# Kernel tuning notes

Hardware: AMD Instinct MI355X
Metric: run time of the kernel (lower is better)

Reference implementation:

```python
import jax, jax.numpy as jnp
import numpy as np

# ---- DNC configuration (mirrors access_config / controller_config / args) ----
T, B, IN, OUT = 64, 32, 64, 64          # time, batch, input_size, output_size
N, Wd, R, NW = 128, 64, 4, 1            # memory_size, word_size, num_reads, num_writes
H = 256                                  # controller hidden_size (2 LSTM layers)
CLIP = 20.0
EPS = 1e-6
NUM_MODES = 2 * NW + 1                   # backward modes, forward modes, content mode
IF_SIZES = [R*Wd, R, NW*Wd, NW, NW*Wd, NW*Wd, R, NW, NW, R*NUM_MODES]
IF_SIZE = int(np.sum(IF_SIZES))


def setup_inputs() -> dict:
    key = jax.random.key(0)
    ks = jax.random.split(key, 12)
    in0 = IN + R * Wd  # controller input = external input + flattened prev reads

    def w(k, shape, fan):
        return jax.random.normal(k, shape, jnp.float32) / np.float32(np.sqrt(fan))

    return {
        "inputs": jax.random.normal(ks[0], (T, B, IN), jnp.float32),
        "Wx0": w(ks[1], (in0, 4 * H), in0),
        "Wh0": w(ks[2], (H, 4 * H), H),
        "b0": jnp.zeros((4 * H,), jnp.float32),
        "Wx1": w(ks[3], (H, 4 * H), H),
        "Wh1": w(ks[4], (H, 4 * H), H),
        "b1": jnp.zeros((4 * H,), jnp.float32),
        "W_if": w(ks[5], (H, IF_SIZE), H),
        "b_if": jnp.zeros((IF_SIZE,), jnp.float32),
        "W_out": w(ks[6], (H + R * Wd, OUT), H + R * Wd),
        "b_out": jnp.zeros((OUT,), jnp.float32),
    }


def _lstm(x, h, c, Wx, Wh, b):
    g = x @ Wx + h @ Wh + b
    i, f, gg, o = jnp.split(g, 4, axis=-1)
    c2 = jax.nn.sigmoid(f) * c + jax.nn.sigmoid(i) * jnp.tanh(gg)
    h2 = jax.nn.sigmoid(o) * jnp.tanh(c2)
    return h2, c2


def _content_weights(memory, keys, strengths):
    # memory [B,N,W], keys [B,h,W], strengths [B,h] -> [B,h,N]
    mnorm = jnp.linalg.norm(memory, axis=-1)          # [B,N]
    knorm = jnp.linalg.norm(keys, axis=-1)            # [B,h]
    dot = jnp.einsum('bhw,bnw->bhn', keys, memory)
    sim = dot / (knorm[..., None] * mnorm[:, None, :] + EPS)
    return jax.nn.softmax(sim * strengths[..., None], axis=-1)


def _allocation(usage):
    # usage [B,N] -> allocation weighting [B,N] (DNC freeness-based)
    usage = EPS + (1.0 - EPS) * usage
    order = jnp.argsort(usage, axis=-1)               # ascending usage (most free first)
    sorted_usage = jnp.take_along_axis(usage, order, axis=-1)
    prod = jnp.cumprod(sorted_usage, axis=-1)
    prod_excl = jnp.concatenate([jnp.ones_like(prod[:, :1]), prod[:, :-1]], axis=-1)
    alloc_sorted = (1.0 - sorted_usage) * prod_excl
    inv = jnp.argsort(order, axis=-1)
    return jnp.take_along_axis(alloc_sorted, inv, axis=-1)


def _dnc_forward(inputs, Wx0, Wh0, b0, Wx1, Wh1, b1, W_if, b_if, W_out, b_out):
    eye = 1.0 - jnp.eye(N, dtype=jnp.float32)
    splits = np.cumsum(IF_SIZES)[:-1]

    def step(state, x_t):
        h0, c0, h1, c1, M, rw, ww, link, prec, usage, reads = state
        ctrl_in = jnp.concatenate([x_t, reads.reshape(B, R * Wd)], axis=-1)
        h0, c0 = _lstm(ctrl_in, h0, c0, Wx0, Wh0, b0)
        h1, c1 = _lstm(h0, h1, c1, Wx1, Wh1, b1)
        ctrl = jnp.clip(h1, -CLIP, CLIP)

        p = jnp.split(ctrl @ W_if + b_if, splits, axis=-1)
        read_keys = p[0].reshape(B, R, Wd)
        read_str = 1.0 + jax.nn.softplus(p[1])              # oneplus
        write_keys = p[2].reshape(B, NW, Wd)
        write_str = 1.0 + jax.nn.softplus(p[3])
        erase = jax.nn.sigmoid(p[4]).reshape(B, NW, Wd)
        write_vec = p[5].reshape(B, NW, Wd)
        free_g = jax.nn.sigmoid(p[6])                       # [B,R]
        alloc_g = jax.nn.sigmoid(p[7])                      # [B,NW]
        write_g = jax.nn.sigmoid(p[8])                      # [B,NW]
        modes = jax.nn.softmax(p[9].reshape(B, R, NUM_MODES), axis=-1)

        # -- usage update (prev write weights, then free gates on prev reads) --
        cw = 1.0 - jnp.prod(1.0 - ww, axis=1)               # [B,N]
        u = usage + (1.0 - usage) * cw
        psi = jnp.prod(1.0 - free_g[..., None] * rw, axis=1)
        usage = u * psi

        # -- write weights: content + allocation, gated --
        wc = _content_weights(M, write_keys, write_str)     # [B,NW,N]
        u_tmp = usage
        ww_heads = []
        for i in range(NW):
            a = _allocation(u_tmp)
            wg = write_g[:, i:i+1]
            ag = alloc_g[:, i:i+1]
            ww_heads.append(wg * (ag * a + (1.0 - ag) * wc[:, i]))
            u_tmp = u_tmp + (1.0 - u_tmp) * wg * a
        ww = jnp.stack(ww_heads, axis=1)                    # [B,NW,N]

        # -- erase + write memory --
        erase_m = jnp.prod(1.0 - ww[..., None] * erase[:, :, None, :], axis=1)  # [B,N,W]
        add_m = jnp.einsum('bwn,bwk->bnk', ww, write_vec)
        M = M * erase_m + add_m

        # -- temporal link matrix + precedence --
        wi = ww[..., :, None]
        wj = ww[..., None, :]
        link = ((1.0 - wi - wj) * link + wi * prec[..., None, :]) * eye
        prec = (1.0 - ww.sum(axis=-1, keepdims=True)) * prec + ww

        # -- read weights: backward / content / forward modes --
        rc = _content_weights(M, read_keys, read_str)       # [B,R,N]
        fwd = jnp.einsum('bwij,brj->brwi', link, rw)
        bwd = jnp.einsum('bwji,brj->brwi', link, rw)
        bmode = modes[..., :NW]
        fmode = modes[..., NW:2*NW]
        cmode = modes[..., 2*NW]
        rw = (jnp.einsum('brw,brwn->brn', bmode, bwd)
              + cmode[..., None] * rc
              + jnp.einsum('brw,brwn->brn', fmode, fwd))
        reads = jnp.einsum('brn,bnk->brk', rw, M)           # [B,R,W]

        out = jnp.clip(jnp.concatenate([ctrl, reads.reshape(B, R * Wd)], axis=-1) @ W_out + b_out,
                       -CLIP, CLIP)
        return (h0, c0, h1, c1, M, rw, ww, link, prec, usage, reads), out

    z = jnp.zeros
    init = (z((B, H)), z((B, H)), z((B, H)), z((B, H)),
            z((B, N, Wd)), z((B, R, N)), z((B, NW, N)),
            z((B, NW, N, N)), z((B, NW, N)), z((B, N)), z((B, R, Wd)))
    _, outs = jax.lax.scan(step, init, inputs)
    return outs                                            # [T,B,OUT]


def reference(inputs, Wx0, Wh0, b0, Wx1, Wh1, b1, W_if, b_if, W_out, b_out):
    return _dnc_forward(inputs, Wx0, Wh0, b0, Wx1, Wh1, b1, W_if, b_if, W_out, b_out)
```

## Files before the change

kernel.cpp:

```cpp
#include <hip/hip_runtime.h>
#include <math.h>


#define TT   64
#define BB   32
#define INW  64
#define OUTW 64
#define NN   128
#define WD   64
#define RR   4
#define HH   256
#define IFSZ 471
#define CLIPV 20.0f
#define EPSV  1e-6f
#define NBLK 96

#define OFF_RK   0
#define OFF_RSTR 256
#define OFF_WK   260
#define OFF_WSTR 324
#define OFF_ER   325
#define OFF_WV   389
#define OFF_FG   453
#define OFF_AG   457
#define OFF_WG   458
#define OFF_MD   459

#define S_WSTR 0
#define S_AG   1
#define S_WG   2
#define S_KNW  3
#define S_WSUM 4
#define S_RSTR 8
#define S_FG   12
#define S_KNR  16
#define S_BM   20
#define S_FM   24
#define S_CM   28

#define A_XS   0
#define A_GL   11840
#define A_C0   12896
#define A_GO   13152
#define A_WS   13216
#define A_WO   34528
#define B_XS   0
#define B_GL   9472
#define B_C1   10528
#define B_W1   10784
#define C_MS   0
#define C_LS   8320
#define C_WW   24832
#define C_PRC  24960
#define C_USG  25088
#define C_RWS  25216
#define C_IFC  25728
#define C_FWD  26208
#define C_BWD  26720
#define C_U2   27232
#define C_WCS  27360
#define C_RCS  27488
#define C_MNO  28000
#define C_RDS  28128
#define C_ERS  28384
#define C_WVS  28448
#define C_SC   28512
#define C_SCAL 28576

#define SMEM_FLOATS 36064
#define SMEM_BYTES  (SMEM_FLOATS*4)

#define W_CTL  0
#define W_RDS  8192
#define W_H0   16384
#define W_H1   32768
#define W_FLA  49152
#define W_FLB  (W_FLA + 1024)
#define W_FLC  (W_FLB + 1024)
#define W_END  (W_FLC + 1024)

__device__ __forceinline__ float sigf(float x){ return 1.0f/(1.0f+expf(-x)); }
__device__ __forceinline__ float sofp(float x){ return fmaxf(x,0.0f)+log1pf(expf(-fabsf(x))); }

__device__ __forceinline__ float gload(const float* p){
  return __hip_atomic_load(p, __ATOMIC_RELAXED, __HIP_MEMORY_SCOPE_AGENT);
}
__device__ __forceinline__ void gstore(float* p, float v){
  __hip_atomic_store(p, v, __ATOMIC_RELAXED, __HIP_MEMORY_SCOPE_AGENT);
}

__device__ __forceinline__ void waitflag(const unsigned* slots, unsigned target){
  if (threadIdx.x < 64){
    for (;;){
      unsigned m = __hip_atomic_load(&slots[(threadIdx.x & 31)*32],
                                     __ATOMIC_RELAXED, __HIP_MEMORY_SCOPE_AGENT);
      #pragma unroll
      for (int s=32;s>0;s>>=1){
        unsigned o = (unsigned)__shfl_xor((int)m, s, 64);
        m = (o < m) ? o : m;
      }
      if (m >= target) break;
      __builtin_amdgcn_s_sleep(2);
    }
  }
  __syncthreads();
}

__device__ __forceinline__ void setflag(unsigned* slots, int g, unsigned val){
  asm volatile("s_waitcnt vmcnt(0)" ::: "memory");
  __syncthreads();
  if (threadIdx.x == 0)
    __hip_atomic_store(&slots[g*32], val, __ATOMIC_RELAXED, __HIP_MEMORY_SCOPE_AGENT);
}

__device__ __forceinline__ float wredSum(float v){
  #pragma unroll
  for (int m=32;m>0;m>>=1) v += __shfl_xor(v,m,64);
  return v;
}
__device__ __forceinline__ float wredMax(float v){
  #pragma unroll
  for (int m=32;m>0;m>>=1) v = fmaxf(v,__shfl_xor(v,m,64));
  return v;
}

__device__ __forceinline__ float bfly64(float (&A)[64], int l, int* jb){
  #pragma unroll
  for (int st=0; st<6; ++st){
    const int m = 1<<st, half = 32>>st;
    const bool hi = (l & m) != 0;
    #pragma unroll
    for (int j=0;j<half;j++){
      float a = A[j], b = A[j+half];
      float keep = hi? b : a;
      float send = hi? a : b;
      A[j] = keep + __shfl_xor(send, m, 64);
    }
  }
  *jb = ((l&1)?32:0)|((l&2)?16:0)|((l&4)?8:0)|((l&8)?4:0)|((l&16)?2:0)|((l&32)?1:0);
  return A[0];
}

#define TILE_FMA(WBASE, WROW, XROW)                                      \
  {                                                                      \
    float xv[8], wv[8];                                                  \
    _Pragma("unroll")                                                    \
    for (int q=0;q<8;q++){                                               \
      wv[q] = sm[(WBASE) + (WROW)*37 + c0 + q];                          \
      xv[q] = Xs[(XROW)*37 + b0 + q];                                    \
    }                                                                    \
    _Pragma("unroll")                                                    \
    for (int bi=0;bi<8;bi++)                                             \
      _Pragma("unroll")                                                  \
      for (int ci=0;ci<8;ci++)                                           \
        acc[bi*8+ci] += xv[bi]*wv[ci];                                   \
  }

extern "C" __global__ __launch_bounds__(1024, 1)
void dnc_coop11(const float* __restrict__ inputs,
                const float* __restrict__ Wx0, const float* __restrict__ Wh0, const float* __restrict__ b0g,
                const float* __restrict__ Wx1, const float* __restrict__ Wh1, const float* __restrict__ b1g,
                const float* __restrict__ Wifg, const float* __restrict__ bifg,
                const float* __restrict__ Woutg, const float* __restrict__ boutg,
                float* __restrict__ outg, float* __restrict__ ws)
{
  const int bid  = blockIdx.x;
  const int role = bid >> 5;
  const int g    = bid & 31;
  const int tid  = threadIdx.x;
  const int lane = tid & 63;
  const int wid  = tid >> 6;

  extern __shared__ float sm[];

  float* gctl  = ws + W_CTL;
  float* greads= ws + W_RDS;
  unsigned* fA = (unsigned*)(ws + W_FLA);
  unsigned* fB = (unsigned*)(ws + W_FLB);
  unsigned* fC = (unsigned*)(ws + W_FLC);

  if (role == 0){
    for (int i = tid; i < 576*32; i += 1024){
      int r = i >> 5, cl = i & 31;
      int cglob = 8*g + (cl&7) + ((cl>>3)<<8);
      float v;
      if (r < 256)      v = Wx0[(64+r)*1024 + cglob];
      else if (r < 320) v = Wx0[(r-256)*1024 + cglob];
      else              v = Wh0[(r-320)*1024 + cglob];
      sm[A_WS + r*37 + cl] = v;
    }
    for (int i = tid; i < 512*2; i += 1024){
      int k = i >> 1, c = i & 1;
      sm[A_WO + k*3 + c] = Woutg[k*64 + 2*g + c];
    }
    if (tid < 256) sm[A_C0 + tid] = 0.0f;
  } else if (role == 1){
    for (int i = tid; i < 512*32; i += 1024){
      int r = i >> 5, cl = i & 31;
      int cglob = 8*g + (cl&7) + ((cl>>3)<<8);
      sm[B_W1 + r*37 + cl] = (r < 256) ? Wx1[r*1024 + cglob]
                                       : Wh1[(r-256)*1024 + cglob];
    }
    if (tid < 256) sm[B_C1 + tid] = 0.0f;
  } else {
    for (int i = tid; i < NN*65;  i += 1024) sm[C_MS + i] = 0.0f;
    for (int i = tid; i < NN*129; i += 1024) sm[C_LS + i] = 0.0f;
    if (tid < 128){ sm[C_WW+tid]=0.f; sm[C_PRC+tid]=0.f; sm[C_USG+tid]=0.f; }
    if (tid < 512) sm[C_RWS+tid]=0.f;
  }
  __syncthreads();

  if (role == 0){
    float* Xs = sm + A_XS;
    for (int t = 0; t <= TT; ++t){
      float* h0old = ws + W_H0 + (t&1)*8192;
      float* h0new = ws + W_H0 + ((t+1)&1)*8192;
      float acc[64]; float accO[16];

      waitflag(fA, (unsigned)t);
      if (t < TT){
        for (int i = tid; i < 256*32; i += 1024){
          int k = i>>5, bb = i&31; Xs[k*37+bb] = gload(&h0old[i]);
        }
        for (int i = tid; i < 64*32; i += 1024){
          int bb = i>>6, k = i&63;
          Xs[(256+k)*37+bb] = inputs[(t*BB + bb)*INW + k];
        }
        __syncthreads();
        #pragma unroll
        for (int j=0;j<64;j++) acc[j]=0.f;
        {
          const int b0 = (wid>>2)*8, c0 = (wid&3)*8;
          #pragma unroll
          for (int i=0;i<4;i++){
            int k = i*64 + lane;
            TILE_FMA(A_WS, 320+k, k)
          }
          TILE_FMA(A_WS, 256+lane, 256+lane)
        }
        __syncthreads();
      }
      if (t > 0){
        waitflag(fB, (unsigned)t);
        for (int i = tid; i < 256*32; i += 1024){
          int k = i>>5, bb = i&31; Xs[k*37+bb] = gload(&gctl[i]);
        }
        __syncthreads();
        #pragma unroll
        for (int j=0;j<16;j++) accO[j]=0.f;
        if (wid < 4){
          const int b0 = wid*8;
          #pragma unroll
          for (int i=0;i<4;i++){
            int k = i*64 + lane;
            float w0 = sm[A_WO + k*3], w1 = sm[A_WO + k*3 + 1];
            float xv[8];
            #pragma unroll
            for (int q=0;q<8;q++) xv[q] = Xs[k*37 + b0 + q];
            #pragma unroll
            for (int bi=0;bi<8;bi++){
              accO[bi*2]   += xv[bi]*w0;
              accO[bi*2+1] += xv[bi]*w1;
            }
          }
        }
        __syncthreads();
      }
      waitflag(fC, (unsigned)t);
      for (int i = tid; i < 256*32; i += 1024){
        int k = i>>5, bb = i&31; Xs[k*37+bb] = gload(&greads[i]);
      }
      __syncthreads();
      if (t < TT){
        {
          const int b0 = (wid>>2)*8, c0 = (wid&3)*8;
          #pragma unroll
          for (int i=0;i<4;i++){
            int k = i*64 + lane;
            TILE_FMA(A_WS, k, k)
          }
          int jb; float v = bfly64(acc, lane, &jb);
          sm[A_GL + (b0 + (jb>>3))*33 + c0 + (jb&7)] = v;
        }
        __syncthreads();
        if (tid < 256){
          int j = tid>>5, bb = tid&31;
          float gi = sm[A_GL + bb*33 + j]      + b0g[8*g + j];
          float gf = sm[A_GL + bb*33 + 8 + j]  + b0g[256 + 8*g + j];
          float gg = sm[A_GL + bb*33 + 16 + j] + b0g[512 + 8*g + j];
          float go = sm[A_GL + bb*33 + 24 + j] + b0g[768 + 8*g + j];
          float c = sigf(gf)*sm[A_C0 + j*32 + bb] + sigf(gi)*tanhf(gg);
          sm[A_C0 + j*32 + bb] = c;
          gstore(&h0new[256*g + tid], sigf(go)*tanhf(c));
        }
        setflag(fA, g, (unsigned)(t+1));
      }
      if (t > 0){
        if (wid < 4){
          const int b0 = wid*8;
          #pragma unroll
          for (int i=0;i<4;i++){
            int k = i*64 + lane;
            float w0 = sm[A_WO + (256+k)*3], w1 = sm[A_WO + (256+k)*3 + 1];
            float xv[8];
            #pragma unroll
            for (int q=0;q<8;q++) xv[q] = Xs[k*37 + b0 + q];
            #pragma unroll
            for (int bi=0;bi<8;bi++){
              accO[bi*2]   += xv[bi]*w0;
              accO[bi*2+1] += xv[bi]*w1;
            }
          }
          #pragma unroll
          for (int st=0; st<4; ++st){
            const int m = 1<<st, half = 8>>st;
            const bool hi = (lane & m) != 0;
            #pragma unroll
            for (int j=0;j<half;j++){
              float a = accO[j], b = accO[j+half];
              float keep = hi? b : a;
              float send = hi? a : b;
              accO[j] = keep + __shfl_xor(send, m, 64);
            }
          }
          accO[0] += __shfl_xor(accO[0], 16, 64);
          accO[0] += __shfl_xor(accO[0], 32, 64);
          int jb = ((lane&1)?8:0)|((lane&2)?4:0)|((lane&4)?2:0)|((lane&8)?1:0);
          if ((lane & 48) == 0){
            int bi = jb>>1, ci = jb&1;
            sm[A_GO + (wid*8+bi)*2 + ci] = accO[0];
          }
        }
        __syncthreads();
        if (tid < 64){
          int bb = tid>>1, c = tid&1;
          float v = sm[A_GO + tid] + boutg[2*g + c];
          outg[((t-1)*BB + bb)*OUTW + 2*g + c] = fminf(CLIPV, fmaxf(-CLIPV, v));
        }
      }
    }
  } else if (role == 1){
    float* Xs = sm + B_XS;
    for (int t = 0; t < TT; ++t){
      float* h0new = ws + W_H0 + ((t+1)&1)*8192;
      float* h1old = ws + W_H1 + (t&1)*8192;
      float* h1new = ws + W_H1 + ((t+1)&1)*8192;
      float acc[64];
      #pragma unroll
      for (int j=0;j<64;j++) acc[j]=0.f;

      waitflag(fB, (unsigned)t);
      for (int i = tid; i < 256*32; i += 1024){
        int k = i>>5, bb = i&31; Xs[k*37+bb] = gload(&h1old[i]);
      }
      __syncthreads();
      {
        const int b0 = (wid>>2)*8, c0 = (wid&3)*8;
        #pragma unroll
        for (int i=0;i<4;i++){
          int k = i*64 + lane;
          TILE_FMA(B_W1, 256+k, k)
        }
      }
      __syncthreads();
      waitflag(fA, (unsigned)(t+1));
      for (int i = tid; i < 256*32; i += 1024){
        int k = i>>5, bb = i&31; Xs[k*37+bb] = gload(&h0new[i]);
      }
      __syncthreads();
      {
        const int b0 = (wid>>2)*8, c0 = (wid&3)*8;
        #pragma unroll
        for (int i=0;i<4;i++){
          int k = i*64 + lane;
          TILE_FMA(B_W1, k, k)
        }
        int jb; float v = bfly64(acc, lane, &jb);
        sm[B_GL + (b0 + (jb>>3))*33 + c0 + (jb&7)] = v;
      }
      __syncthreads();
      if (tid < 256){
        int j = tid>>5, bb = tid&31;
        float gi = sm[B_GL + bb*33 + j]      + b1g[8*g + j];
        float gf = sm[B_GL + bb*33 + 8 + j]  + b1g[256 + 8*g + j];
        float gg = sm[B_GL + bb*33 + 16 + j] + b1g[512 + 8*g + j];
        float go = sm[B_GL + bb*33 + 24 + j] + b1g[768 + 8*g + j];
        float c = sigf(gf)*sm[B_C1 + j*32 + bb] + sigf(gi)*tanhf(gg);
        sm[B_C1 + j*32 + bb] = c;
        float h = sigf(go)*tanhf(c);
        gstore(&h1new[256*g + tid], h);
        gstore(&gctl[256*g + tid], fminf(CLIPV, fmaxf(-CLIPV, h)));
      }
      setflag(fB, g, (unsigned)(t+1));
    }
  } else {
    float* Ms  = sm + C_MS;
    float* Ls  = sm + C_LS;
    float* wws = sm + C_WW;
    float* prc = sm + C_PRC;
    float* usg = sm + C_USG;
    float* rws = sm + C_RWS;
    float* ifcl= sm + C_IFC;
    float* fwds= sm + C_FWD;
    float* bwds= sm + C_BWD;
    float* u2  = sm + C_U2;
    float* wcs = sm + C_WCS;
    float* rcs = sm + C_RCS;
    float* mno = sm + C_MNO;
    float* ers = sm + C_ERS;
    float* wvs = sm + C_WVS;
    float* sc  = sm + C_SC;
    float* scal= sm + C_SCAL;
    float* ctl_l = sm + C_RCS;
    float* part  = sm + C_FWD;

    for (int t = 0; t < TT; ++t){
      if (tid < 128){
        float s=0.f;
        #pragma unroll 8
        for (int d=0;d<WD;d++){ float v=Ms[tid*65+d]; s+=v*v; }
        mno[tid]=sqrtf(s);
      }
      waitflag(fB, (unsigned)(t+1));
      if (tid < 256) ctl_l[tid] = gload(&gctl[tid*32 + g]);
      __syncthreads();
      {
        const int kq = tid >> 9, c = tid & 511;
        if (c < IFSZ){
          const float* Wp = Wifg + (size_t)(kq*128)*IFSZ + c;
          const float* xp = ctl_l + kq*128;
          float a0=0.f, a1=0.f;
          #pragma unroll 8
          for (int k=0;k<128;k+=2){
            a0 += xp[k]   * Wp[(size_t)k*IFSZ];
            a1 += xp[k+1] * Wp[(size_t)(k+1)*IFSZ];
          }
          part[kq*512 + c] = a0 + a1;
        }
      }
      __syncthreads();
      if (tid < IFSZ) ifcl[tid] = part[tid] + part[512+tid] + bifg[tid];
      __syncthreads();

      if (tid < RR){
        scal[S_RSTR+tid]=1.0f+sofp(ifcl[OFF_RSTR+tid]);
        scal[S_FG+tid]  =sigf(ifcl[OFF_FG+tid]);
        float m0=ifcl[OFF_MD+tid*3], m1=ifcl[OFF_MD+tid*3+1], m2=ifcl[OFF_MD+tid*3+2];
        float mx=fmaxf(m0,fmaxf(m1,m2));
        float e0=expf(m0-mx), e1=expf(m1-mx), e2=expf(m2-mx);
        float s=e0+e1+e2;
        scal[S_BM+tid]=e0/s; scal[S_FM+tid]=e1/s; scal[S_CM+tid]=e2/s;
      }
      if (tid == 4) scal[S_WSTR]=1.0f+sofp(ifcl[OFF_WSTR]);
      if (tid == 5) scal[S_AG]=sigf(ifcl[OFF_AG]);
      if (tid == 6) scal[S_WG]=sigf(ifcl[OFF_WG]);
      if (tid >= 64 && tid < 128){
        int d=tid-64;
        ers[d]=sigf(ifcl[OFF_ER+d]);
        wvs[d]=ifcl[OFF_WV+d];
      }
      if (wid == 8){
        float v=ifcl[OFF_WK+lane]; float s=wredSum(v*v);
        if (lane==0) scal[S_KNW]=sqrtf(s);
      }
      if (wid >= 10 && wid < 14){
        int r=wid-10; float v=ifcl[OFF_RK+r*WD+lane]; float s=wredSum(v*v);
        if (lane==0) scal[S_KNR+r]=sqrtf(s);
      }
      __syncthreads();
      if (tid < NN){
        float dot=0.f;
        #pragma unroll 8
        for (int d=0;d<WD;d++) dot += ifcl[OFF_WK+d]*Ms[tid*65+d];
        float sim = dot/(scal[S_KNW]*mno[tid]+EPSV);
        wcs[tid]=sim*scal[S_WSTR];
      }
      __syncthreads();
      if (tid < NN){ float mx=wredMax(wcs[tid]); if(lane==0) sc[wid]=mx; }
      __syncthreads();
      if (tid < NN){
        float mx=fmaxf(sc[0],sc[1]);
        float e=expf(wcs[tid]-mx);
        wcs[tid]=e;
        float s=wredSum(e); if(lane==0) sc[2+wid]=s;
      }
      __syncthreads();
      if (tid < NN) wcs[tid]=wcs[tid]/(sc[2]+sc[3]);
      __syncthreads();
      if (tid < NN){
        float cw = wws[tid];
        float u  = usg[tid] + (1.0f-usg[tid])*cw;
        float psi=1.0f;
        #pragma unroll
        for (int r=0;r<RR;r++) psi *= 1.0f - scal[S_FG+r]*rws[r*NN+tid];
        float us = u*psi;
        usg[tid]=us;
        u2[tid] = EPSV + (1.0f-EPSV)*us;
      }
      __syncthreads();
      if (tid < NN){
        float ui=u2[tid]; float p=1.0f;
        for (int j=0;j<NN;j++){
          float uj=u2[j];
          bool take = (uj<ui) || (uj==ui && j<tid);
          p *= take ? uj : 1.0f;
        }
        float a = (1.0f-ui)*p;
        float wwn = scal[S_WG]*( scal[S_AG]*a + (1.0f-scal[S_AG])*wcs[tid] );
        wws[tid]=wwn;
        float s=wredSum(wwn); if(lane==0) sc[wid]=s;
      }
      __syncthreads();
      if (tid==0) scal[S_WSUM]=sc[0]+sc[1];
      __syncthreads();
      #pragma unroll
      for (int i=0;i<8;i++){
        int el=tid+i*1024, n=el>>6, d=el&63;
        float w=wws[n];
        Ms[n*65+d] = Ms[n*65+d]*(1.0f - w*ers[d]) + w*wvs[d];
      }
      #pragma unroll
      for (int i=0;i<16;i++){
        int el=tid+i*1024, li=el>>7, lj=el&127;
        float v = (li==lj) ? 0.0f
                : (1.0f - wws[li] - wws[lj])*Ls[li*129+lj] + wws[li]*prc[lj];
        Ls[li*129+lj]=v;
      }
      __syncthreads();
      if (tid < NN) prc[tid] = (1.0f - scal[S_WSUM])*prc[tid] + wws[tid];
      if (tid >= 128 && tid < 256){
        int n=tid-128; float s=0.f;
        #pragma unroll 8
        for (int d=0;d<WD;d++){ float v=Ms[n*65+d]; s+=v*v; }
        mno[n]=sqrtf(s);
      }
      __syncthreads();
      if (tid < RR*NN){
        int r=tid>>7, n=tid&127;
        float dot=0.f;
        #pragma unroll 8
        for (int d=0;d<WD;d++) dot += ifcl[OFF_RK+r*WD+d]*Ms[n*65+d];
        float sim = dot/(scal[S_KNR+r]*mno[n]+EPSV);
        rcs[tid]=sim*scal[S_RSTR+r];
      }
      __syncthreads();
      if (tid < RR*NN){ float mx=wredMax(rcs[tid]); if(lane==0) sc[wid]=mx; }
      __syncthreads();
      if (tid < RR*NN){
        int r=tid>>7;
        float mx=fmaxf(sc[r*2],sc[r*2+1]);
        float e=expf(rcs[tid]-mx);
        rcs[tid]=e;
        float s=wredSum(e); if(lane==0) sc[8+wid]=s;
      }
      __syncthreads();
      if (tid < RR*NN){
        int r=tid>>7;
        rcs[tid]=rcs[tid]/(sc[8+r*2]+sc[9+r*2]);
      }
      __syncthreads();
      if (tid < RR*NN){
        int r=tid>>7, i=tid&127;
        float f=0.f, bw=0.f;
        const float* rwr = rws + r*NN;
        #pragma unroll 4
        for (int j=0;j<NN;j++){
          float rv=rwr[j];
          f  += Ls[i*129+j]*rv;
          bw += Ls[j*129+i]*rv;
        }
        fwds[tid]=f; bwds[tid]=bw;
      }
      __syncthreads();
      if (tid < RR*NN){
        int r=tid>>7;
        rws[tid] = scal[S_BM+r]*bwds[tid] + scal[S_CM+r]*rcs[tid] + scal[S_FM+r]*fwds[tid];
      }
      __syncthreads();
      if (tid < RR*WD){
        int r=tid>>6, d=tid&63;
        float s=0.f;
        #pragma unroll 8
        for (int n=0;n<NN;n++) s += rws[r*NN+n]*Ms[n*65+d];
        gstore(&greads[tid*32 + g], s);
      }
      setflag(fC, g, (unsigned)(t+1));
    }
  }
}

extern "C" void kernel_launch(void* const* d_in, const int* in_sizes, int n_in,
                              void* d_out, int out_size, void* d_ws, size_t ws_size,
                              hipStream_t stream)
{
  const float* inputs=(const float*)d_in[0];
  const float* Wx0   =(const float*)d_in[1];
  const float* Wh0   =(const float*)d_in[2];
  const float* b0    =(const float*)d_in[3];
  const float* Wx1   =(const float*)d_in[4];
  const float* Wh1   =(const float*)d_in[5];
  const float* b1    =(const float*)d_in[6];
  const float* Wif   =(const float*)d_in[7];
  const float* bif   =(const float*)d_in[8];
  const float* Wout  =(const float*)d_in[9];
  const float* bout  =(const float*)d_in[10];
  float* out = (float*)d_out;
  float* ws  = (float*)d_ws;

  hipMemsetAsync(ws, 0, W_END * sizeof(float), stream);

  hipFuncSetAttribute((const void*)dnc_coop11,
                      hipFuncAttributeMaxDynamicSharedMemorySize, SMEM_BYTES);

  void* args[] = { (void*)&inputs, (void*)&Wx0, (void*)&Wh0, (void*)&b0,
                   (void*)&Wx1, (void*)&Wh1, (void*)&b1, (void*)&Wif,
                   (void*)&bif, (void*)&Wout, (void*)&bout, (void*)&out,
                   (void*)&ws };
  hipLaunchCooperativeKernel((void*)dnc_coop11, dim3(NBLK), dim3(1024),
                             args, SMEM_BYTES, stream);
}
```

Measured before the change: 3.135 ms.

## Merge memory-stage phases to cut barriers and rebalance per-step work

Restructures the per-timestep memory block. It splits the interface matvec into four k-quarters over all 1024 threads. The usage update now runs alongside write content scoring, and the read content scoring (with the memory norm fused in) runs concurrently with the link forward/backward products. The softmax normalisations are folded into their consumers, and the final read-vector reduction is split four ways over all threads. The aim is to remove many __syncthreads phases and idle threads on the serial critical path, at the cost of an extra reduction buffer and some redundant norm computation.

```diff
diff --git a/kernel.cpp b/kernel.cpp
--- a/kernel.cpp
+++ b/kernel.cpp
@@ -30,7 +30,6 @@
 #define S_AG   1
 #define S_WG   2
 #define S_KNW  3
-#define S_WSUM 4
 #define S_RSTR 8
 #define S_FG   12
 #define S_KNR  16
@@ -61,11 +60,11 @@
 #define C_WCS  27360
 #define C_RCS  27488
 #define C_MNO  28000
-#define C_RDS  28128
 #define C_ERS  28384
 #define C_WVS  28448
 #define C_SC   28512
 #define C_SCAL 28576
+#define C_PART2 28608
 
 #define SMEM_FLOATS 36064
 #define SMEM_BYTES  (SMEM_FLOATS*4)
@@ -157,7 +156,7 @@
   }
 
 extern "C" __global__ __launch_bounds__(1024, 1)
-void dnc_coop11(const float* __restrict__ inputs,
+void dnc_coop12(const float* __restrict__ inputs,
                 const float* __restrict__ Wx0, const float* __restrict__ Wh0, const float* __restrict__ b0g,
                 const float* __restrict__ Wx1, const float* __restrict__ Wh1, const float* __restrict__ b1g,
                 const float* __restrict__ Wifg, const float* __restrict__ bifg,
@@ -412,7 +411,7 @@
     float* sc  = sm + C_SC;
     float* scal= sm + C_SCAL;
     float* ctl_l = sm + C_RCS;
-    float* part  = sm + C_FWD;
+    float* part2 = sm + C_PART2;
 
     for (int t = 0; t < TT; ++t){
       if (tid < 128){
@@ -425,21 +424,24 @@
       if (tid < 256) ctl_l[tid] = gload(&gctl[tid*32 + g]);
       __syncthreads();
       {
-        const int kq = tid >> 9, c = tid & 511;
-        if (c < IFSZ){
-          const float* Wp = Wifg + (size_t)(kq*128)*IFSZ + c;
-          const float* xp = ctl_l + kq*128;
-          float a0=0.f, a1=0.f;
-          #pragma unroll 8
-          for (int k=0;k<128;k+=2){
-            a0 += xp[k]   * Wp[(size_t)k*IFSZ];
-            a1 += xp[k+1] * Wp[(size_t)(k+1)*IFSZ];
-          }
-          part[kq*512 + c] = a0 + a1;
-        }
-      }
-      __syncthreads();
-      if (tid < IFSZ) ifcl[tid] = part[tid] + part[512+tid] + bifg[tid];
+        const int kq = tid >> 8, c = tid & 255;
+        const int c2 = c + 256;
+        const bool has2 = (c2 < IFSZ);
+        const float* Wp = Wifg + (size_t)(kq*64)*IFSZ;
+        const float* xp = ctl_l + kq*64;
+        float a0=0.f, a1=0.f;
+        #pragma unroll 8
+        for (int k=0;k<64;k++){
+          float x = xp[k];
+          a0 += x * Wp[(size_t)k*IFSZ + c];
+          if (has2) a1 += x * Wp[(size_t)k*IFSZ + c2];
+        }
+        part2[kq*512 + c] = a0;
+        if (has2) part2[kq*512 + c2] = a1;
+      }
+      __syncthreads();
+      if (tid < IFSZ)
+        ifcl[tid] = part2[tid] + part2[512+tid] + part2[1024+tid] + part2[1536+tid] + bifg[tid];
       __syncthreads();
 
       if (tid < RR){
@@ -468,12 +470,22 @@
         if (lane==0) scal[S_KNR+r]=sqrtf(s);
       }
       __syncthreads();
+
       if (tid < NN){
         float dot=0.f;
         #pragma unroll 8
         for (int d=0;d<WD;d++) dot += ifcl[OFF_WK+d]*Ms[tid*65+d];
-        float sim = dot/(scal[S_KNW]*mno[tid]+EPSV);
-        wcs[tid]=sim*scal[S_WSTR];
+        wcs[tid] = dot/(scal[S_KNW]*mno[tid]+EPSV)*scal[S_WSTR];
+      } else if (tid < 256){
+        int n = tid-128;
+        float cw = wws[n];
+        float u  = usg[n] + (1.0f-usg[n])*cw;
+        float psi=1.0f;
+        #pragma unroll
+        for (int r=0;r<RR;r++) psi *= 1.0f - scal[S_FG+r]*rws[r*NN+n];
+        float us = u*psi;
+        usg[n]=us;
+        u2[n] = EPSV + (1.0f-EPSV)*us;
       }
       __syncthreads();
       if (tid < NN){ float mx=wredMax(wcs[tid]); if(lane==0) sc[wid]=mx; }
@@ -485,20 +497,8 @@
         float s=wredSum(e); if(lane==0) sc[2+wid]=s;
       }
       __syncthreads();
-      if (tid < NN) wcs[tid]=wcs[tid]/(sc[2]+sc[3]);
-      __syncthreads();
       if (tid < NN){
-        float cw = wws[tid];
-        float u  = usg[tid] + (1.0f-usg[tid])*cw;
-        float psi=1.0f;
-        #pragma unroll
-        for (int r=0;r<RR;r++) psi *= 1.0f - scal[S_FG+r]*rws[r*NN+tid];
-        float us = u*psi;
-        usg[tid]=us;
-        u2[tid] = EPSV + (1.0f-EPSV)*us;
-      }
-      __syncthreads();
-      if (tid < NN){
+        float wcsum = sc[2]+sc[3];
         float ui=u2[tid]; float p=1.0f;
         for (int j=0;j<NN;j++){
           float uj=u2[j];
@@ -506,12 +506,10 @@
           p *= take ? uj : 1.0f;
         }
         float a = (1.0f-ui)*p;
-        float wwn = scal[S_WG]*( scal[S_AG]*a + (1.0f-scal[S_AG])*wcs[tid] );
+        float wwn = scal[S_WG]*( scal[S_AG]*a + (1.0f-scal[S_AG])*(wcs[tid]/wcsum) );
         wws[tid]=wwn;
-        float s=wredSum(wwn); if(lane==0) sc[wid]=s;
-      }
-      __syncthreads();
-      if (tid==0) scal[S_WSUM]=sc[0]+sc[1];
+        float s=wredSum(wwn); if(lane==0) sc[4+wid]=s;
+      }
       __syncthreads();
       #pragma unroll
       for (int i=0;i<8;i++){
@@ -527,40 +525,18 @@
         Ls[li*129+lj]=v;
       }
       __syncthreads();
-      if (tid < NN) prc[tid] = (1.0f - scal[S_WSUM])*prc[tid] + wws[tid];
-      if (tid >= 128 && tid < 256){
-        int n=tid-128; float s=0.f;
+      if (tid < 512){
+        int r=tid>>7, n=tid&127;
+        float dot=0.f, q=0.f;
         #pragma unroll 8
-        for (int d=0;d<WD;d++){ float v=Ms[n*65+d]; s+=v*v; }
-        mno[n]=sqrtf(s);
-      }
-      __syncthreads();
-      if (tid < RR*NN){
-        int r=tid>>7, n=tid&127;
-        float dot=0.f;
-        #pragma unroll 8
-        for (int d=0;d<WD;d++) dot += ifcl[OFF_RK+r*WD+d]*Ms[n*65+d];
-        float sim = dot/(scal[S_KNR+r]*mno[n]+EPSV);
-        rcs[tid]=sim*scal[S_RSTR+r];
-      }
-      __syncthreads();
-      if (tid < RR*NN){ float mx=wredMax(rcs[tid]); if(lane==0) sc[wid]=mx; }
-      __syncthreads();
-      if (tid < RR*NN){
-        int r=tid>>7;
-        float mx=fmaxf(sc[r*2],sc[r*2+1]);
-        float e=expf(rcs[tid]-mx);
-        rcs[tid]=e;
-        float s=wredSum(e); if(lane==0) sc[8+wid]=s;
-      }
-      __syncthreads();
-      if (tid < RR*NN){
-        int r=tid>>7;
-        rcs[tid]=rcs[tid]/(sc[8+r*2]+sc[9+r*2]);
-      }
-      __syncthreads();
-      if (tid < RR*NN){
-        int r=tid>>7, i=tid&127;
+        for (int d=0;d<WD;d++){
+          float m = Ms[n*65+d];
+          dot += ifcl[OFF_RK+r*WD+d]*m;
+          q   += m*m;
+        }
+        rcs[tid] = dot/(scal[S_KNR+r]*sqrtf(q)+EPSV)*scal[S_RSTR+r];
+      } else {
+        int idx=tid-512, r=idx>>7, i=idx&127;
         float f=0.f, bw=0.f;
         const float* rwr = rws + r*NN;
         #pragma unroll 4
@@ -569,19 +545,41 @@
           f  += Ls[i*129+j]*rv;
           bw += Ls[j*129+i]*rv;
         }
-        fwds[tid]=f; bwds[tid]=bw;
-      }
-      __syncthreads();
-      if (tid < RR*NN){
+        fwds[idx]=f; bwds[idx]=bw;
+      }
+      __syncthreads();
+      if (tid < 512){ float mx=wredMax(rcs[tid]); if(lane==0) sc[8+wid]=mx; }
+      __syncthreads();
+      if (tid < 512){
         int r=tid>>7;
-        rws[tid] = scal[S_BM+r]*bwds[tid] + scal[S_CM+r]*rcs[tid] + scal[S_FM+r]*fwds[tid];
-      }
-      __syncthreads();
-      if (tid < RR*WD){
-        int r=tid>>6, d=tid&63;
+        float mx=fmaxf(sc[8+r*2],sc[9+r*2]);
+        float e=expf(rcs[tid]-mx);
+        rcs[tid]=e;
+        float s=wredSum(e); if(lane==0) sc[16+wid]=s;
+      }
+      __syncthreads();
+      if (tid < 512){
+        int r=tid>>7;
+        float rsum = sc[16+r*2]+sc[17+r*2];
+        rws[tid] = scal[S_BM+r]*bwds[tid] + scal[S_CM+r]*(rcs[tid]/rsum) + scal[S_FM+r]*fwds[tid];
+      } else if (tid < 640){
+        int n = tid-512;
+        float wsm = sc[4]+sc[5];
+        prc[n] = (1.0f - wsm)*prc[n] + wws[n];
+      }
+      __syncthreads();
+      {
+        int kq=tid>>8, j=tid&255, r=j>>6, d=j&63;
         float s=0.f;
+        const float* rwr = rws + r*NN + kq*32;
+        const float* mp  = Ms + (kq*32)*65 + d;
         #pragma unroll 8
-        for (int n=0;n<NN;n++) s += rws[r*NN+n]*Ms[n*65+d];
+        for (int n=0;n<32;n++) s += rwr[n]*mp[n*65];
+        part2[kq*256 + j] = s;
+      }
+      __syncthreads();
+      if (tid < 256){
+        float s = part2[tid]+part2[256+tid]+part2[512+tid]+part2[768+tid];
         gstore(&greads[tid*32 + g], s);
       }
       setflag(fC, g, (unsigned)(t+1));
@@ -609,13 +607,13 @@
 
   hipMemsetAsync(ws, 0, W_END * sizeof(float), stream);
 
-  hipFuncSetAttribute((const void*)dnc_coop11,
+  hipFuncSetAttribute((const void*)dnc_coop12,
                       hipFuncAttributeMaxDynamicSharedMemorySize, SMEM_BYTES);
 
   void* args[] = { (void*)&inputs, (void*)&Wx0, (void*)&Wh0, (void*)&b0,
                    (void*)&Wx1, (void*)&Wh1, (void*)&b1, (void*)&Wif,
                    (void*)&bif, (void*)&Wout, (void*)&bout, (void*)&out,
                    (void*)&ws };
-  hipLaunchCooperativeKernel((void*)dnc_coop11, dim3(NBLK), dim3(1024),
+  hipLaunchCooperativeKernel((void*)dnc_coop12, dim3(NBLK), dim3(1024),
                              args, SMEM_BYTES, stream);
 }
```

After: 3.007 ms. -4.1%, faster.
